# Kernel optimization log

Hardware: AMD Instinct MI355X
Metric: run time of the kernel (lower is better)

Reference implementation:

```python
import jax, jax.numpy as jnp
import numpy as np

DIM = 192
NH = 4
B, H, W = 4, 128, 128


def _conv1x1(x, w, b):
    # x: [b,c,h,w], w: [o,c], b: [o]
    return jnp.einsum('oc,bchw->bohw', w, x) + b[None, :, None, None]


def _dwconv3(x, w, b):
    # depthwise 3x3, w: [C,1,3,3]
    y = jax.lax.conv_general_dilated(
        x, w, window_strides=(1, 1), padding='SAME',
        feature_group_count=x.shape[1],
        dimension_numbers=('NCHW', 'OIHW', 'NCHW'))
    return y + b[None, :, None, None]


def _to_heads(x, nh):
    b, c, h, w = x.shape
    return x.reshape(b, nh, c // nh, h * w)  # b head c (hw)


def _l2norm(x):
    # torch F.normalize(dim=-1): x / max(||x||, eps)
    n = jnp.sqrt(jnp.sum(x * x, axis=-1, keepdims=True))
    return x / jnp.maximum(n, 1e-12)


def _chan_attn(q, k, v, temp):
    # q,k,v: [b,head,c,n]; temp: [head,1,1] -> broadcasts over [b,head,c,c]
    scores = jnp.einsum('bhcn,bhdn->bhcd', q, k) * temp
    a = jax.nn.softmax(scores, axis=-1)
    return jnp.einsum('bhcd,bhdn->bhcn', a, v)


def setup_inputs() -> dict:
    key = jax.random.key(0)
    ks = jax.random.split(key, 16)
    d3 = 3 * DIM
    inp = {
        'sar': jax.random.normal(ks[0], (B, DIM, H, W), jnp.float32),
        'ms': jax.random.normal(ks[1], (B, DIM, H, W), jnp.float32),
        'ms_qkv_w': jax.random.normal(ks[2], (d3, DIM), jnp.float32) * 0.02,
        'ms_qkv_b': jnp.zeros((d3,), jnp.float32),
        'ms_dw_w': jax.random.normal(ks[3], (d3, 1, 3, 3), jnp.float32) * 0.1,
        'ms_dw_b': jnp.zeros((d3,), jnp.float32),
        'ms_temp': jnp.ones((NH, 1, 1), jnp.float32),
        'sar_qkv_w': jax.random.normal(ks[4], (d3, DIM), jnp.float32) * 0.02,
        'sar_qkv_b': jnp.zeros((d3,), jnp.float32),
        'sar_dw_w': jax.random.normal(ks[5], (d3, 1, 3, 3), jnp.float32) * 0.1,
        'sar_dw_b': jnp.zeros((d3,), jnp.float32),
        'sar_temp': jnp.ones((NH, 1, 1), jnp.float32),
        'ms_proj_w': jax.random.normal(ks[6], (DIM, 2 * DIM), jnp.float32) * 0.02,
        'ms_proj_b': jnp.zeros((DIM,), jnp.float32),
        'sar_proj_w': jax.random.normal(ks[7], (DIM, DIM), jnp.float32) * 0.02,
        'sar_proj_b': jnp.zeros((DIM,), jnp.float32),
    }
    return inp


def reference(sar, ms, ms_qkv_w, ms_qkv_b, ms_dw_w, ms_dw_b, ms_temp,
              sar_qkv_w, sar_qkv_b, sar_dw_w, sar_dw_b, sar_temp,
              ms_proj_w, ms_proj_b, sar_proj_w, sar_proj_b):
    b, c, h, w = ms.shape

    ms_qkv = _dwconv3(_conv1x1(ms, ms_qkv_w, ms_qkv_b), ms_dw_w, ms_dw_b)
    ms_q, ms_k, ms_v = jnp.split(ms_qkv, 3, axis=1)
    ms_q = _l2norm(_to_heads(ms_q, NH))
    ms_k = _l2norm(_to_heads(ms_k, NH))
    ms_v = _to_heads(ms_v, NH)

    sar_qkv = _dwconv3(_conv1x1(sar, sar_qkv_w, sar_qkv_b), sar_dw_w, sar_dw_b)
    sar_q, sar_k, sar_v = jnp.split(sar_qkv, 3, axis=1)
    sar_q = _l2norm(_to_heads(sar_q, NH))
    sar_k = _l2norm(_to_heads(sar_k, NH))
    sar_v = _to_heads(sar_v, NH)

    ms_self = _chan_attn(ms_q, ms_k, ms_v, ms_temp).reshape(b, c, h, w)
    sar_self = _chan_attn(sar_q, sar_k, sar_v, sar_temp).reshape(b, c, h, w)
    cross = _chan_attn(sar_q, ms_k, sar_v, ms_temp).reshape(b, c, h, w)

    sar_out = sar + _conv1x1(sar_self, sar_proj_w, sar_proj_b)
    ms_cat = jnp.concatenate([ms_self, cross + ms_self], axis=1)
    ms_out = ms + _conv1x1(ms_cat, ms_proj_w, ms_proj_b)
    return (sar_out, ms_out)
```

## Files before the change

kernel.cpp:

```cpp
#include <hip/hip_runtime.h>
#include <hip/hip_bf16.h>
#include <cstdint>

#define DIMC 192
#define BB 4
#define NN 16384
#define D3 576
#define CHD 48
#define WWID 128
#define HHGT 128

typedef short short8 __attribute__((ext_vector_type(8)));
typedef float f32x4 __attribute__((ext_vector_type(4)));

union FragU { uint4 u4; short8 s8; };

__device__ __forceinline__ float bf2f(uint16_t v) {
    return __uint_as_float(((uint32_t)v) << 16);
}
__device__ __forceinline__ float2 upk2(uint32_t u) {
    float2 r;
    r.x = __uint_as_float(u << 16);
    r.y = __uint_as_float(u & 0xffff0000u);
    return r;
}
__device__ __forceinline__ uint16_t f2bf(float f) {
    uint32_t x = __float_as_uint(f);
    return (uint16_t)((x + 0x7fffu + ((x >> 16) & 1u)) >> 16);
}
__device__ __forceinline__ uint4 pack8(const uint16_t* v) {
    uint4 u;
    u.x = (uint32_t)v[0] | ((uint32_t)v[1] << 16);
    u.y = (uint32_t)v[2] | ((uint32_t)v[3] << 16);
    u.z = (uint32_t)v[4] | ((uint32_t)v[5] << 16);
    u.w = (uint32_t)v[6] | ((uint32_t)v[7] << 16);
    return u;
}

__global__ __launch_bounds__(256) void k_prep(
    const float* __restrict__ w0, const float* __restrict__ w1,
    const float* __restrict__ w2, const float* __restrict__ w3,
    uint16_t* __restrict__ o0, uint16_t* __restrict__ o1,
    uint16_t* __restrict__ o2a, uint16_t* __restrict__ o2b,
    uint16_t* __restrict__ o3)
{
    int i = blockIdx.x * 256 + threadIdx.x;
    if (i < 110592) { o0[i] = f2bf(w0[i]); return; }
    i -= 110592;
    if (i < 110592) { o1[i] = f2bf(w1[i]); return; }
    i -= 110592;
    if (i < 36864) {
        const int o = i / DIMC, c = i % DIMC;
        o2a[i] = f2bf(w2[o * 384 + c] + w2[o * 384 + DIMC + c]);
        o2b[i] = f2bf(w2[o * 384 + DIMC + c]);
        return;
    }
    i -= 36864;
    if (i < 36864) o3[i] = f2bf(w3[i]);
}

__global__ __launch_bounds__(256, 2) void k_conv_mfma(
    const float* __restrict__ x, const uint16_t* __restrict__ wbf,
    const float* __restrict__ bias, uint16_t* __restrict__ out)
{
    __shared__ uint16_t xs[128][200];
    __shared__ uint16_t wst[64][200];
    const int t = threadIdx.x;
    const int nb = blockIdx.x & 127;
    const int b = blockIdx.x >> 7;
    const int n0 = nb * 128;

    const int lane = t & 63, wvid = t >> 6;
    const int lm = lane & 15, g = lane >> 4;
    const int wm = wvid >> 1, wn = wvid & 1;

    {
        const int sn = t & 127, kh = t >> 7;
        const float* xcol = x + ((size_t)b * DIMC + kh * 96) * NN + n0 + sn;
        for (int u = 0; u < 12; ++u) {
            uint16_t vals[8];
#pragma unroll
            for (int j = 0; j < 8; ++j)
                vals[j] = f2bf(xcol[(size_t)(u * 8 + j) * NN]);
            *(uint4*)&xs[sn][(kh * 12 + u) * 8] = pack8(vals);
        }
    }
    {
        const int wm_ = t >> 2, wq = t & 3;
        const uint16_t* wrow = wbf + (size_t)wm_ * DIMC;
#pragma unroll
        for (int i = 0; i < 6; ++i) {
            const int unit = i * 4 + wq;
            *(uint4*)&wst[wm_][unit * 8] = *(const uint4*)&wrow[unit * 8];
        }
    }
    __syncthreads();

    FragU bfr[6][4];
#pragma unroll
    for (int ks = 0; ks < 6; ++ks)
#pragma unroll
        for (int nj = 0; nj < 4; ++nj) {
            const int row = wn * 64 + nj * 16 + lm;
            bfr[ks][nj].u4 = *(const uint4*)&xs[row][ks * 32 + g * 8];
        }

    for (int mb = 0; mb < 9; ++mb) {
        if (mb) {
            __syncthreads();
            const int wm_ = t >> 2, wq = t & 3;
            const uint16_t* wrow = wbf + (size_t)(mb * 64 + wm_) * DIMC;
#pragma unroll
            for (int i = 0; i < 6; ++i) {
                const int unit = i * 4 + wq;
                *(uint4*)&wst[wm_][unit * 8] = *(const uint4*)&wrow[unit * 8];
            }
            __syncthreads();
        }
        f32x4 acc[2][4];
#pragma unroll
        for (int mi = 0; mi < 2; ++mi)
#pragma unroll
            for (int nj = 0; nj < 4; ++nj) acc[mi][nj] = (f32x4){0.f, 0.f, 0.f, 0.f};
#pragma unroll
        for (int ks = 0; ks < 6; ++ks) {
            FragU afr[2];
#pragma unroll
            for (int mi = 0; mi < 2; ++mi) {
                const int row = wm * 32 + mi * 16 + lm;
                afr[mi].u4 = *(const uint4*)&wst[row][ks * 32 + g * 8];
            }
#pragma unroll
            for (int mi = 0; mi < 2; ++mi)
#pragma unroll
                for (int nj = 0; nj < 4; ++nj)
                    acc[mi][nj] = __builtin_amdgcn_mfma_f32_16x16x32_bf16(
                        afr[mi].s8, bfr[ks][nj].s8, acc[mi][nj], 0, 0, 0);
        }
#pragma unroll
        for (int mi = 0; mi < 2; ++mi) {
            const int rbase = mb * 64 + wm * 32 + mi * 16 + g * 4;
            const float4 bv = *(const float4*)&bias[rbase];
            const float bva[4] = {bv.x, bv.y, bv.z, bv.w};
#pragma unroll
            for (int nj = 0; nj < 4; ++nj) {
                const int gcol = n0 + wn * 64 + nj * 16 + lm;
#pragma unroll
                for (int r = 0; r < 4; ++r)
                    out[((size_t)b * D3 + rbase + r) * NN + gcol] =
                        f2bf(acc[mi][nj][r] + bva[r]);
            }
        }
    }
}

template<int PHASES>
__global__ __launch_bounds__(256, 2) void k_proj_mfma(
    const uint16_t* __restrict__ x0, const uint16_t* __restrict__ x1,
    const uint16_t* __restrict__ w0, const uint16_t* __restrict__ w1,
    const float* __restrict__ bias, const float* __restrict__ resid,
    float* __restrict__ out)
{
    __shared__ uint16_t xs[128][200];
    __shared__ uint16_t wst[64][200];
    const int t = threadIdx.x;
    const int nb = blockIdx.x & 127;
    const int b = blockIdx.x >> 7;
    const int n0 = nb * 128;

    const int lane = t & 63, wvid = t >> 6;
    const int lm = lane & 15, g = lane >> 4;
    const int wm = wvid >> 1, wn = wvid & 1;

    f32x4 acc[3][2][4];
#pragma unroll
    for (int mb = 0; mb < 3; ++mb)
#pragma unroll
        for (int mi = 0; mi < 2; ++mi)
#pragma unroll
            for (int nj = 0; nj < 4; ++nj) acc[mb][mi][nj] = (f32x4){0.f, 0.f, 0.f, 0.f};

    for (int ph = 0; ph < PHASES; ++ph) {
        const uint16_t* xsrc = ph ? x1 : x0;
        const uint16_t* wsrc = ph ? w1 : w0;
        if (ph) __syncthreads();
        {
            const int sn = t & 127, kh = t >> 7;
            const uint16_t* xcol = xsrc + ((size_t)b * DIMC + kh * 96) * NN + n0 + sn;
            for (int u = 0; u < 12; ++u) {
                uint16_t vals[8];
#pragma unroll
                for (int j = 0; j < 8; ++j)
                    vals[j] = xcol[(size_t)(u * 8 + j) * NN];
                *(uint4*)&xs[sn][(kh * 12 + u) * 8] = pack8(vals);
            }
        }
        {
            const int wm_ = t >> 2, wq = t & 3;
            const uint16_t* wrow = wsrc + (size_t)wm_ * DIMC;
#pragma unroll
            for (int i = 0; i < 6; ++i) {
                const int unit = i * 4 + wq;
                *(uint4*)&wst[wm_][unit * 8] = *(const uint4*)&wrow[unit * 8];
            }
        }
        __syncthreads();
        FragU bfr[6][4];
#pragma unroll
        for (int ks = 0; ks < 6; ++ks)
#pragma unroll
            for (int nj = 0; nj < 4; ++nj) {
                const int row = wn * 64 + nj * 16 + lm;
                bfr[ks][nj].u4 = *(const uint4*)&xs[row][ks * 32 + g * 8];
            }
        for (int mb = 0; mb < 3; ++mb) {
            if (mb) {
                __syncthreads();
                const int wm_ = t >> 2, wq = t & 3;
                const uint16_t* wrow = wsrc + (size_t)(mb * 64 + wm_) * DIMC;
#pragma unroll
                for (int i = 0; i < 6; ++i) {
                    const int unit = i * 4 + wq;
                    *(uint4*)&wst[wm_][unit * 8] = *(const uint4*)&wrow[unit * 8];
                }
                __syncthreads();
            }
#pragma unroll
            for (int ks = 0; ks < 6; ++ks) {
                FragU afr[2];
#pragma unroll
                for (int mi = 0; mi < 2; ++mi) {
                    const int row = wm * 32 + mi * 16 + lm;
                    afr[mi].u4 = *(const uint4*)&wst[row][ks * 32 + g * 8];
                }
#pragma unroll
                for (int mi = 0; mi < 2; ++mi)
#pragma unroll
                    for (int nj = 0; nj < 4; ++nj)
                        acc[mb][mi][nj] = __builtin_amdgcn_mfma_f32_16x16x32_bf16(
                            afr[mi].s8, bfr[ks][nj].s8, acc[mb][mi][nj], 0, 0, 0);
            }
        }
    }
#pragma unroll
    for (int mb = 0; mb < 3; ++mb)
#pragma unroll
        for (int mi = 0; mi < 2; ++mi) {
            const int rbase = mb * 64 + wm * 32 + mi * 16 + g * 4;
            const float4 bv = *(const float4*)&bias[rbase];
            const float bva[4] = {bv.x, bv.y, bv.z, bv.w};
#pragma unroll
            for (int nj = 0; nj < 4; ++nj) {
                const int gcol = n0 + wn * 64 + nj * 16 + lm;
#pragma unroll
                for (int r = 0; r < 4; ++r) {
                    const size_t idx = ((size_t)b * DIMC + rbase + r) * NN + gcol;
                    out[idx] = resid[idx] + acc[mb][mi][nj][r] + bva[r];
                }
            }
        }
}

__global__ __launch_bounds__(256) void k_dwconv2(
    const uint16_t* __restrict__ in, const float* __restrict__ w9,
    const float* __restrict__ bias, uint16_t* __restrict__ out)
{
    const int t = threadIdx.x;
    const int bc = blockIdx.z;
    const int ch = bc % D3;
    const int xg = t & 15, yl = t >> 4;
    const int x0 = xg * 8;
    const int y = blockIdx.y * 16 + yl;
    const uint16_t* p = in + (size_t)bc * NN;
    float wv[9];
#pragma unroll
    for (int k = 0; k < 9; ++k) wv[k] = w9[ch * 9 + k];
    float r[3][10];
#pragma unroll
    for (int dy = 0; dy < 3; ++dy) {
        const int yy = y + dy - 1;
        if (yy < 0 || yy >= HHGT) {
#pragma unroll
            for (int j = 0; j < 10; ++j) r[dy][j] = 0.f;
        } else {
            const uint16_t* row = p + yy * WWID;
            uint4 u = *(const uint4*)(row + x0);
            const uint16_t* pv = (const uint16_t*)&u;
#pragma unroll
            for (int j = 0; j < 8; ++j) r[dy][j + 1] = bf2f(pv[j]);
            r[dy][0] = (x0 > 0) ? bf2f(row[x0 - 1]) : 0.f;
            r[dy][9] = (x0 + 8 < WWID) ? bf2f(row[x0 + 8]) : 0.f;
        }
    }
    const float base = bias[ch];
    uint16_t ov[8];
#pragma unroll
    for (int j = 0; j < 8; ++j) {
        float a = base;
#pragma unroll
        for (int dy = 0; dy < 3; ++dy)
#pragma unroll
            for (int dx = 0; dx < 3; ++dx)
                a = fmaf(r[dy][j + dx], wv[dy * 3 + dx], a);
        ov[j] = f2bf(a);
    }
    *(uint4*)(out + (size_t)bc * NN + y * WWID + x0) = pack8(ov);
}

__global__ __launch_bounds__(256) void k_scores_mfma(
    const uint16_t* __restrict__ qkv_ms, const uint16_t* __restrict__ qkv_sar,
    float* __restrict__ partial, float* __restrict__ sumsq)
{
    const int t = threadIdx.x;
    const int bid = blockIdx.x;
    const int ck = bid & 15;
    const int pid = bid >> 4;
    const int h = pid & 3, b = pid >> 2;
    const int n0 = ck * 1024;
    const int lane = t & 63, w = t >> 6;

    const uint16_t* qm  = qkv_ms  + ((size_t)b * D3 + h * CHD) * NN;
    const uint16_t* km  = qkv_ms  + ((size_t)b * D3 + DIMC + h * CHD) * NN;
    const uint16_t* qsr = qkv_sar + ((size_t)b * D3 + h * CHD) * NN;
    const uint16_t* ksr = qkv_sar + ((size_t)b * D3 + DIMC + h * CHD) * NN;

    if (w < 3) {
        const uint16_t* qb = (w == 0) ? qm : qsr;
        const uint16_t* kb = (w == 1) ? ksr : km;
        const int lm = lane & 15, g = lane >> 4;
        f32x4 acc[3][3];
#pragma unroll
        for (int i = 0; i < 3; ++i)
#pragma unroll
            for (int j = 0; j < 3; ++j) acc[i][j] = (f32x4){0.f, 0.f, 0.f, 0.f};
        for (int kk = 0; kk < 32; ++kk) {
            const int nb2 = n0 + kk * 32 + g * 8;
            FragU qf[3], kf[3];
#pragma unroll
            for (int i = 0; i < 3; ++i)
                qf[i].u4 = *(const uint4*)&qb[(size_t)(i * 16 + lm) * NN + nb2];
#pragma unroll
            for (int j = 0; j < 3; ++j)
                kf[j].u4 = *(const uint4*)&kb[(size_t)(j * 16 + lm) * NN + nb2];
#pragma unroll
            for (int i = 0; i < 3; ++i)
#pragma unroll
                for (int j = 0; j < 3; ++j)
                    acc[i][j] = __builtin_amdgcn_mfma_f32_16x16x32_bf16(
                        qf[i].s8, kf[j].s8, acc[i][j], 0, 0, 0);
        }
        float* pd = partial + (((size_t)pid * 3 + w) * 16 + ck) * 2304;
        const int g4 = g * 4;
#pragma unroll
        for (int i = 0; i < 3; ++i)
#pragma unroll
            for (int j = 0; j < 3; ++j)
#pragma unroll
                for (int r = 0; r < 4; ++r)
                    pd[(i * 16 + g4 + r) * 48 + j * 16 + lm] = acc[i][j][r];
    } else {
#pragma unroll
        for (int rep = 0; rep < 3; ++rep) {
            const int rid = rep * 64 + lane;
            const int s = rid / CHD, c = rid % CHD;
            const uint16_t* rowp =
                (s == 0) ? qm  + (size_t)c * NN :
                (s == 1) ? km  + (size_t)c * NN :
                (s == 2) ? qsr + (size_t)c * NN :
                           ksr + (size_t)c * NN;
            float sum = 0.f;
            for (int u = 0; u < 128; ++u) {
                uint4 v = *(const uint4*)&rowp[n0 + u * 8];
                uint32_t uu[4] = {v.x, v.y, v.z, v.w};
#pragma unroll
                for (int q = 0; q < 4; ++q) {
                    float2 f = upk2(uu[q]);
                    sum = fmaf(f.x, f.x, fmaf(f.y, f.y, sum));
                }
            }
            sumsq[(((size_t)pid * 16 + ck) * 4 + s) * CHD + c] = sum;
        }
    }
}

__global__ __launch_bounds__(64) void k_softmax(
    const float* __restrict__ partial, const float* __restrict__ sumsq,
    const float* __restrict__ ms_temp, const float* __restrict__ sar_temp,
    float* __restrict__ A)
{
    const int lane = threadIdx.x;
    const int bi = blockIdx.x;
    const int c = bi % 48;
    const int pid = bi / 48;
    const int h = pid & 3, b = (pid >> 2) & 3, type = pid >> 4;
    const int pid16 = b * 4 + h;
    float s;
    if (lane < 48) {
        float accv = 0.f;
        const float* pp = partial + ((size_t)pid16 * 3 + type) * 16 * 2304 + c * 48 + lane;
#pragma unroll
        for (int ck = 0; ck < 16; ++ck) accv += pp[(size_t)ck * 2304];
        const int qset = (type == 0) ? 0 : 2;
        const int kset = (type == 1) ? 3 : 1;
        float qsum = 0.f, ksum = 0.f;
        const float* sq = sumsq + (size_t)pid16 * 16 * 4 * CHD;
#pragma unroll
        for (int ck = 0; ck < 16; ++ck) {
            qsum += sq[ck * 4 * CHD + qset * CHD + c];
            ksum += sq[ck * 4 * CHD + kset * CHD + lane];
        }
        const float tval = (type == 1) ? sar_temp[h] : ms_temp[h];
        const float qsc = 1.0f / fmaxf(sqrtf(qsum), 1e-12f);
        const float ksc = 1.0f / fmaxf(sqrtf(ksum), 1e-12f);
        s = accv * qsc * ksc * tval;
    } else {
        s = -3.0e38f;
    }
    float m = s;
#pragma unroll
    for (int o = 32; o > 0; o >>= 1) m = fmaxf(m, __shfl_xor(m, o));
    float e = (lane < 48) ? __expf(s - m) : 0.f;
    float sum = e;
#pragma unroll
    for (int o = 32; o > 0; o >>= 1) sum += __shfl_xor(sum, o);
    if (lane < 48) A[(size_t)pid * 2304 + c * 48 + lane] = e / sum;
}

__global__ __launch_bounds__(256) void k_apply_mfma(
    const float* __restrict__ A, const uint16_t* __restrict__ qkv_ms,
    const uint16_t* __restrict__ qkv_sar, uint16_t* __restrict__ attn)
{
    __shared__ uint16_t vs[256][40];
    __shared__ uint16_t as[48][40];
    const int t = threadIdx.x;
    const int nb = blockIdx.x & 63;
    const int pid = blockIdx.x >> 6;
    const int h = pid & 3, b = (pid >> 2) & 3, type = pid >> 4;
    const int n0 = nb * 256;
    const uint16_t* vsrc = (type == 0) ? qkv_ms : qkv_sar;
    const uint16_t* vb = vsrc + ((size_t)b * D3 + 2 * DIMC + (size_t)h * CHD) * NN;
    const float* Ap = A + (size_t)pid * 2304;

    const int lane = t & 63, wvid = t >> 6;
    const int lm = lane & 15, g = lane >> 4;

    f32x4 acc[3][4];
#pragma unroll
    for (int i = 0; i < 3; ++i)
#pragma unroll
        for (int j = 0; j < 4; ++j) acc[i][j] = (f32x4){0.f, 0.f, 0.f, 0.f};

    for (int k0 = 0; k0 < 64; k0 += 32) {
        __syncthreads();
#pragma unroll
        for (int kh = 0; kh < 2; ++kh) {
            uint16_t vals[16];
#pragma unroll
            for (int j = 0; j < 16; ++j) {
                const int d = k0 + kh * 16 + j;
                vals[j] = (d < CHD) ? vb[(size_t)d * NN + n0 + t] : (uint16_t)0;
            }
            const int u0 = (2 * kh) ^ ((t >> 3) & 3);
            const int u1 = (2 * kh + 1) ^ ((t >> 3) & 3);
            *(uint4*)&vs[t][u0 * 8] = pack8(&vals[0]);
            *(uint4*)&vs[t][u1 * 8] = pack8(&vals[8]);
        }
        if (t < 192) {
            const int c = t >> 2, dq = t & 3;
            uint16_t av[8];
#pragma unroll
            for (int i = 0; i < 8; ++i) {
                const int d = k0 + dq * 8 + i;
                av[i] = (d < CHD) ? f2bf(Ap[c * CHD + d]) : (uint16_t)0;
            }
            const int u = dq ^ ((c >> 3) & 3);
            *(uint4*)&as[c][u * 8] = pack8(av);
        }
        __syncthreads();
        FragU afr[3], bfr[4];
#pragma unroll
        for (int mi = 0; mi < 3; ++mi) {
            const int row = mi * 16 + lm;
            afr[mi].u4 = *(const uint4*)&as[row][(g ^ ((row >> 3) & 3)) * 8];
        }
#pragma unroll
        for (int nj = 0; nj < 4; ++nj) {
            const int row = wvid * 64 + nj * 16 + lm;
            bfr[nj].u4 = *(const uint4*)&vs[row][(g ^ ((row >> 3) & 3)) * 8];
        }
#pragma unroll
        for (int mi = 0; mi < 3; ++mi)
#pragma unroll
            for (int nj = 0; nj < 4; ++nj)
                acc[mi][nj] = __builtin_amdgcn_mfma_f32_16x16x32_bf16(
                    afr[mi].s8, bfr[nj].s8, acc[mi][nj], 0, 0, 0);
    }

    uint16_t* ob = attn + (size_t)type * BB * DIMC * NN +
                   ((size_t)b * DIMC + (size_t)h * CHD) * NN;
#pragma unroll
    for (int mi = 0; mi < 3; ++mi) {
        const int rbase = mi * 16 + g * 4;
#pragma unroll
        for (int nj = 0; nj < 4; ++nj) {
            const int gcol = n0 + wvid * 64 + nj * 16 + lm;
#pragma unroll
            for (int r = 0; r < 4; ++r)
                ob[(size_t)(rbase + r) * NN + gcol] = f2bf(acc[mi][nj][r]);
        }
    }
}

extern "C" void kernel_launch(void* const* d_in, const int* in_sizes, int n_in,
                              void* d_out, int out_size, void* d_ws, size_t ws_size,
                              hipStream_t stream)
{
    const float* sar        = (const float*)d_in[0];
    const float* ms         = (const float*)d_in[1];
    const float* ms_qkv_w   = (const float*)d_in[2];
    const float* ms_qkv_b   = (const float*)d_in[3];
    const float* ms_dw_w    = (const float*)d_in[4];
    const float* ms_dw_b    = (const float*)d_in[5];
    const float* ms_temp    = (const float*)d_in[6];
    const float* sar_qkv_w  = (const float*)d_in[7];
    const float* sar_qkv_b  = (const float*)d_in[8];
    const float* sar_dw_w   = (const float*)d_in[9];
    const float* sar_dw_b   = (const float*)d_in[10];
    const float* sar_temp   = (const float*)d_in[11];
    const float* ms_proj_w  = (const float*)d_in[12];
    const float* ms_proj_b  = (const float*)d_in[13];
    const float* sar_proj_w = (const float*)d_in[14];
    const float* sar_proj_b = (const float*)d_in[15];

    char* ws = (char*)d_ws;
    uint16_t* tmp     = (uint16_t*)(ws);
    uint16_t* qkv_ms  = (uint16_t*)(ws + 75497472ull);
    uint16_t* qkv_sar = (uint16_t*)(ws + 150994944ull);
    float* partial    = (float*)(ws);
    float* sumsq      = (float*)(ws + 8388608ull);
    float* Amat       = (float*)(ws + 230043648ull);
    uint16_t* wq_ms   = (uint16_t*)(ws + 230486016ull);
    uint16_t* wq_sar  = (uint16_t*)(ws + 230707200ull);
    uint16_t* wp1_ms  = (uint16_t*)(ws + 230928384ull);
    uint16_t* wp2_ms  = (uint16_t*)(ws + 231002112ull);
    uint16_t* wp_sar  = (uint16_t*)(ws + 231075840ull);
    uint16_t* attn    = tmp;

    float* out_sar = (float*)d_out;
    float* out_ms  = out_sar + (size_t)BB * DIMC * NN;

    dim3 b256(256);
    k_prep<<<dim3(1152), b256, 0, stream>>>(ms_qkv_w, sar_qkv_w, ms_proj_w, sar_proj_w,
                                            wq_ms, wq_sar, wp1_ms, wp2_ms, wp_sar);
    k_conv_mfma<<<dim3(128 * BB), b256, 0, stream>>>(ms, wq_ms, ms_qkv_b, tmp);
    k_dwconv2<<<dim3(1, 8, BB * D3), b256, 0, stream>>>(tmp, ms_dw_w, ms_dw_b, qkv_ms);
    k_conv_mfma<<<dim3(128 * BB), b256, 0, stream>>>(sar, wq_sar, sar_qkv_b, tmp);
    k_dwconv2<<<dim3(1, 8, BB * D3), b256, 0, stream>>>(tmp, sar_dw_w, sar_dw_b, qkv_sar);

    k_scores_mfma<<<dim3(256), b256, 0, stream>>>(qkv_ms, qkv_sar, partial, sumsq);
    k_softmax<<<dim3(48 * 48), dim3(64), 0, stream>>>(partial, sumsq, ms_temp, sar_temp, Amat);
    k_apply_mfma<<<dim3(48 * 64), b256, 0, stream>>>(Amat, qkv_ms, qkv_sar, attn);

    uint16_t* ms_self  = attn;
    uint16_t* sar_self = attn + (size_t)BB * DIMC * NN;
    uint16_t* crossb   = attn + 2ull * BB * DIMC * NN;
    k_proj_mfma<1><<<dim3(128 * BB), b256, 0, stream>>>(
        sar_self, nullptr, wp_sar, nullptr, sar_proj_b, sar, out_sar);
    k_proj_mfma<2><<<dim3(128 * BB), b256, 0, stream>>>(
        ms_self, crossb, wp1_ms, wp2_ms, ms_proj_b, ms, out_ms);
}
```

Baseline: 311.7 us.

## Split scores reduction over more chunks and prefetch weights into registers

The scores kernel now splits the spatial reduction into 64 chunks of 256 instead of 16 chunks of 1024. This raises the grid from 256 to 1024 blocks so more CUs stay busy, at the cost of more partial sums for the softmax kernel to read and add. The 1x1 conv and projection kernels now prefetch the next 64-row weight slab into registers while the current MFMA block runs, then write it to shared memory. This hides global load latency but adds register pressure.

```diff
diff --git a/kernel.cpp b/kernel.cpp
--- a/kernel.cpp
+++ b/kernel.cpp
@@ -9,6 +9,8 @@
 #define CHD 48
 #define WWID 128
 #define HHGT 128
+#define NCK 64
+#define CKW 256
 
 typedef short short8 __attribute__((ext_vector_type(8)));
 typedef float f32x4 __attribute__((ext_vector_type(4)));
@@ -73,7 +75,15 @@
     const int lane = t & 63, wvid = t >> 6;
     const int lm = lane & 15, g = lane >> 4;
     const int wm = wvid >> 1, wn = wvid & 1;
-
+    const int wm_ = t >> 2, wq = t & 3;
+
+    uint4 wreg[6];
+    {
+        const uint16_t* wrow = wbf + (size_t)wm_ * DIMC;
+#pragma unroll
+        for (int i = 0; i < 6; ++i)
+            wreg[i] = *(const uint4*)&wrow[(i * 4 + wq) * 8];
+    }
     {
         const int sn = t & 127, kh = t >> 7;
         const float* xcol = x + ((size_t)b * DIMC + kh * 96) * NN + n0 + sn;
@@ -85,15 +95,9 @@
             *(uint4*)&xs[sn][(kh * 12 + u) * 8] = pack8(vals);
         }
     }
-    {
-        const int wm_ = t >> 2, wq = t & 3;
-        const uint16_t* wrow = wbf + (size_t)wm_ * DIMC;
-#pragma unroll
-        for (int i = 0; i < 6; ++i) {
-            const int unit = i * 4 + wq;
-            *(uint4*)&wst[wm_][unit * 8] = *(const uint4*)&wrow[unit * 8];
-        }
-    }
+#pragma unroll
+    for (int i = 0; i < 6; ++i)
+        *(uint4*)&wst[wm_][(i * 4 + wq) * 8] = wreg[i];
     __syncthreads();
 
     FragU bfr[6][4];
@@ -106,16 +110,11 @@
         }
 
     for (int mb = 0; mb < 9; ++mb) {
-        if (mb) {
-            __syncthreads();
-            const int wm_ = t >> 2, wq = t & 3;
-            const uint16_t* wrow = wbf + (size_t)(mb * 64 + wm_) * DIMC;
-#pragma unroll
-            for (int i = 0; i < 6; ++i) {
-                const int unit = i * 4 + wq;
-                *(uint4*)&wst[wm_][unit * 8] = *(const uint4*)&wrow[unit * 8];
-            }
-            __syncthreads();
+        if (mb < 8) {
+            const uint16_t* wrow = wbf + (size_t)((mb + 1) * 64 + wm_) * DIMC;
+#pragma unroll
+            for (int i = 0; i < 6; ++i)
+                wreg[i] = *(const uint4*)&wrow[(i * 4 + wq) * 8];
         }
         f32x4 acc[2][4];
 #pragma unroll
@@ -150,6 +149,13 @@
                     out[((size_t)b * D3 + rbase + r) * NN + gcol] =
                         f2bf(acc[mi][nj][r] + bva[r]);
             }
+        }
+        if (mb < 8) {
+            __syncthreads();
+#pragma unroll
+            for (int i = 0; i < 6; ++i)
+                *(uint4*)&wst[wm_][(i * 4 + wq) * 8] = wreg[i];
+            __syncthreads();
         }
     }
 }
@@ -171,6 +177,7 @@
     const int lane = t & 63, wvid = t >> 6;
     const int lm = lane & 15, g = lane >> 4;
     const int wm = wvid >> 1, wn = wvid & 1;
+    const int wm_ = t >> 2, wq = t & 3;
 
     f32x4 acc[3][2][4];
 #pragma unroll
@@ -184,6 +191,13 @@
         const uint16_t* xsrc = ph ? x1 : x0;
         const uint16_t* wsrc = ph ? w1 : w0;
         if (ph) __syncthreads();
+        uint4 wreg[6];
+        {
+            const uint16_t* wrow = wsrc + (size_t)wm_ * DIMC;
+#pragma unroll
+            for (int i = 0; i < 6; ++i)
+                wreg[i] = *(const uint4*)&wrow[(i * 4 + wq) * 8];
+        }
         {
             const int sn = t & 127, kh = t >> 7;
             const uint16_t* xcol = xsrc + ((size_t)b * DIMC + kh * 96) * NN + n0 + sn;
@@ -195,15 +209,9 @@
                 *(uint4*)&xs[sn][(kh * 12 + u) * 8] = pack8(vals);
             }
         }
-        {
-            const int wm_ = t >> 2, wq = t & 3;
-            const uint16_t* wrow = wsrc + (size_t)wm_ * DIMC;
-#pragma unroll
-            for (int i = 0; i < 6; ++i) {
-                const int unit = i * 4 + wq;
-                *(uint4*)&wst[wm_][unit * 8] = *(const uint4*)&wrow[unit * 8];
-            }
-        }
+#pragma unroll
+        for (int i = 0; i < 6; ++i)
+            *(uint4*)&wst[wm_][(i * 4 + wq) * 8] = wreg[i];
         __syncthreads();
         FragU bfr[6][4];
 #pragma unroll
@@ -214,16 +222,11 @@
                 bfr[ks][nj].u4 = *(const uint4*)&xs[row][ks * 32 + g * 8];
             }
         for (int mb = 0; mb < 3; ++mb) {
-            if (mb) {
-                __syncthreads();
-                const int wm_ = t >> 2, wq = t & 3;
-                const uint16_t* wrow = wsrc + (size_t)(mb * 64 + wm_) * DIMC;
-#pragma unroll
-                for (int i = 0; i < 6; ++i) {
-                    const int unit = i * 4 + wq;
-                    *(uint4*)&wst[wm_][unit * 8] = *(const uint4*)&wrow[unit * 8];
-                }
-                __syncthreads();
+            if (mb < 2) {
+                const uint16_t* wrow = wsrc + (size_t)((mb + 1) * 64 + wm_) * DIMC;
+#pragma unroll
+                for (int i = 0; i < 6; ++i)
+                    wreg[i] = *(const uint4*)&wrow[(i * 4 + wq) * 8];
             }
 #pragma unroll
             for (int ks = 0; ks < 6; ++ks) {
@@ -239,6 +242,13 @@
                     for (int nj = 0; nj < 4; ++nj)
                         acc[mb][mi][nj] = __builtin_amdgcn_mfma_f32_16x16x32_bf16(
                             afr[mi].s8, bfr[ks][nj].s8, acc[mb][mi][nj], 0, 0, 0);
+            }
+            if (mb < 2) {
+                __syncthreads();
+#pragma unroll
+                for (int i = 0; i < 6; ++i)
+                    *(uint4*)&wst[wm_][(i * 4 + wq) * 8] = wreg[i];
+                __syncthreads();
             }
         }
     }
@@ -313,10 +323,10 @@
 {
     const int t = threadIdx.x;
     const int bid = blockIdx.x;
-    const int ck = bid & 15;
-    const int pid = bid >> 4;
+    const int ck = bid & (NCK - 1);
+    const int pid = bid / NCK;
     const int h = pid & 3, b = pid >> 2;
-    const int n0 = ck * 1024;
+    const int n0 = ck * CKW;
     const int lane = t & 63, w = t >> 6;
 
     const uint16_t* qm  = qkv_ms  + ((size_t)b * D3 + h * CHD) * NN;
@@ -333,7 +343,8 @@
         for (int i = 0; i < 3; ++i)
 #pragma unroll
             for (int j = 0; j < 3; ++j) acc[i][j] = (f32x4){0.f, 0.f, 0.f, 0.f};
-        for (int kk = 0; kk < 32; ++kk) {
+#pragma unroll 2
+        for (int kk = 0; kk < CKW / 32; ++kk) {
             const int nb2 = n0 + kk * 32 + g * 8;
             FragU qf[3], kf[3];
 #pragma unroll
@@ -349,7 +360,7 @@
                     acc[i][j] = __builtin_amdgcn_mfma_f32_16x16x32_bf16(
                         qf[i].s8, kf[j].s8, acc[i][j], 0, 0, 0);
         }
-        float* pd = partial + (((size_t)pid * 3 + w) * 16 + ck) * 2304;
+        float* pd = partial + (((size_t)pid * 3 + w) * NCK + ck) * 2304;
         const int g4 = g * 4;
 #pragma unroll
         for (int i = 0; i < 3; ++i)
@@ -369,7 +380,8 @@
                 (s == 2) ? qsr + (size_t)c * NN :
                            ksr + (size_t)c * NN;
             float sum = 0.f;
-            for (int u = 0; u < 128; ++u) {
+#pragma unroll 4
+            for (int u = 0; u < CKW / 8; ++u) {
                 uint4 v = *(const uint4*)&rowp[n0 + u * 8];
                 uint32_t uu[4] = {v.x, v.y, v.z, v.w};
 #pragma unroll
@@ -378,7 +390,7 @@
                     sum = fmaf(f.x, f.x, fmaf(f.y, f.y, sum));
                 }
             }
-            sumsq[(((size_t)pid * 16 + ck) * 4 + s) * CHD + c] = sum;
+            sumsq[(((size_t)pid * NCK + ck) * 4 + s) * CHD + c] = sum;
         }
     }
 }
@@ -397,15 +409,15 @@
     float s;
     if (lane < 48) {
         float accv = 0.f;
-        const float* pp = partial + ((size_t)pid16 * 3 + type) * 16 * 2304 + c * 48 + lane;
-#pragma unroll
-        for (int ck = 0; ck < 16; ++ck) accv += pp[(size_t)ck * 2304];
+        const float* pp = partial + ((size_t)pid16 * 3 + type) * NCK * 2304 + c * 48 + lane;
+#pragma unroll 8
+        for (int ck = 0; ck < NCK; ++ck) accv += pp[(size_t)ck * 2304];
         const int qset = (type == 0) ? 0 : 2;
         const int kset = (type == 1) ? 3 : 1;
         float qsum = 0.f, ksum = 0.f;
-        const float* sq = sumsq + (size_t)pid16 * 16 * 4 * CHD;
-#pragma unroll
-        for (int ck = 0; ck < 16; ++ck) {
+        const float* sq = sumsq + (size_t)pid16 * NCK * 4 * CHD;
+#pragma unroll 8
+        for (int ck = 0; ck < NCK; ++ck) {
             qsum += sq[ck * 4 * CHD + qset * CHD + c];
             ksum += sq[ck * 4 * CHD + kset * CHD + lane];
         }
@@ -537,7 +549,7 @@
     uint16_t* qkv_ms  = (uint16_t*)(ws + 75497472ull);
     uint16_t* qkv_sar = (uint16_t*)(ws + 150994944ull);
     float* partial    = (float*)(ws);
-    float* sumsq      = (float*)(ws + 8388608ull);
+    float* sumsq      = (float*)(ws + 33554432ull);
     float* Amat       = (float*)(ws + 230043648ull);
     uint16_t* wq_ms   = (uint16_t*)(ws + 230486016ull);
     uint16_t* wq_sar  = (uint16_t*)(ws + 230707200ull);
@@ -557,7 +569,7 @@
     k_conv_mfma<<<dim3(128 * BB), b256, 0, stream>>>(sar, wq_sar, sar_qkv_b, tmp);
     k_dwconv2<<<dim3(1, 8, BB * D3), b256, 0, stream>>>(tmp, sar_dw_w, sar_dw_b, qkv_sar);
 
-    k_scores_mfma<<<dim3(256), b256, 0, stream>>>(qkv_ms, qkv_sar, partial, sumsq);
+    k_scores_mfma<<<dim3(16 * NCK), b256, 0, stream>>>(qkv_ms, qkv_sar, partial, sumsq);
     k_softmax<<<dim3(48 * 48), dim3(64), 0, stream>>>(partial, sumsq, ms_temp, sar_temp, Amat);
     k_apply_mfma<<<dim3(48 * 64), b256, 0, stream>>>(Amat, qkv_ms, qkv_sar, attn);
 
```

Measured after the change: 398.0 us. 1.28x slower.
